# Performance work log

Hardware: AMD Instinct MI355X
Metric: run time of the kernel (lower is better)

## Reference

```python
import jax, jax.numpy as jnp
import numpy as np

B, SQ, SKV, D, H = 2, 2048, 2048, 1024, 16
DH = D // H


def setup_inputs() -> dict:
    key = jax.random.key(0)
    ks = jax.random.split(key, 4)
    s = 0.02
    return {
        "query_input": jax.random.normal(ks[0], (B, SQ, D), jnp.float32),
        "kv_input": jax.random.normal(ks[1], (B, SKV, D), jnp.float32),
        "Wq": jax.random.normal(ks[2], (D, D), jnp.float32) * s,
        "bq": jnp.zeros((D,), jnp.float32),
        "Wkv": jax.random.normal(ks[3], (D, 2 * D), jnp.float32) * s,
        "bkv": jnp.zeros((2 * D,), jnp.float32),
        "Wo": jax.random.normal(jax.random.fold_in(key, 7), (D, D), jnp.float32) * s,
        "bo": jnp.zeros((D,), jnp.float32),
    }


def reference(query_input, kv_input, Wq, bq, Wkv, bkv, Wo, bo):
    scale = 1.0 / jnp.sqrt(jnp.float32(DH))
    # Projections
    q = query_input @ Wq + bq                      # [B, SQ, D]
    kv = kv_input @ Wkv + bkv                      # [B, SKV, 2D]
    k, v = jnp.split(kv, 2, axis=-1)               # [B, SKV, D] each
    # Split heads: [B, H, S, DH]
    q = q.reshape(B, SQ, H, DH).transpose(0, 2, 1, 3)
    k = k.reshape(B, SKV, H, DH).transpose(0, 2, 1, 3)
    v = v.reshape(B, SKV, H, DH).transpose(0, 2, 1, 3)
    # Scores S = QK^T / sqrt(d_k)
    scores = jnp.einsum("bhqd,bhkd->bhqk", q, k) * scale
    attn = jax.nn.softmax(scores, axis=-1)
    out = jnp.einsum("bhqk,bhkd->bhqd", attn, v)   # [B, H, SQ, DH]
    out = out.transpose(0, 2, 1, 3).reshape(B, SQ, D)
    return out @ Wo + bo
```

## Files before the change

### kernel.cpp

```cpp
#include <hip/hip_runtime.h>

typedef unsigned short u16;
typedef unsigned int u32;
typedef __bf16 bf16x8 __attribute__((ext_vector_type(8)));
typedef __bf16 bf16x2 __attribute__((ext_vector_type(2)));
typedef float f32x4 __attribute__((ext_vector_type(4)));

#define QSCALE 0.18033688011112f

__device__ __forceinline__ u16 f2bf(float f) {
  u32 u = __builtin_bit_cast(u32, f);
  u += 0x7fffu + ((u >> 16) & 1u);
  return (u16)(u >> 16);
}

__device__ __forceinline__ u32 pkbf(float a, float b) {
  bf16x2 t = {(__bf16)a, (__bf16)b};
  return __builtin_bit_cast(u32, t);
}

__device__ __forceinline__ float bf2f(u16 x) {
  u32 u = (u32)x << 16;
  return __builtin_bit_cast(float, u);
}

__device__ __forceinline__ bf16x8 as_bf16x8(uint4 v) {
  return __builtin_bit_cast(bf16x8, v);
}

__device__ __forceinline__ void async16(const void* g, void* l) {
  __builtin_amdgcn_global_load_lds(
      (__attribute__((address_space(1))) void*)(g),
      (__attribute__((address_space(3))) void*)(l), 16, 0, 0);
}

__global__ void prep_kernel(const float* __restrict__ xq, const float* __restrict__ xkv,
                            const float* __restrict__ Wq, const float* __restrict__ Wkv,
                            const float* __restrict__ Wo,
                            u16* __restrict__ Xq16, u16* __restrict__ Xkv16,
                            u16* __restrict__ WqT, u16* __restrict__ WkvT,
                            u16* __restrict__ WoT) {
  const int bid = blockIdx.x, tid = threadIdx.x;
  if (bid < 8192) {
    int i = bid * 256 + tid;
    const float* s; u16* d; int j;
    if (i < 1048576) { s = xq; d = Xq16; j = i; }
    else             { s = xkv; d = Xkv16; j = i - 1048576; }
    float4 v = ((const float4*)s)[j];
    ushort4 o;
    o.x = f2bf(v.x); o.y = f2bf(v.y); o.z = f2bf(v.z); o.w = f2bf(v.w);
    ((ushort4*)d)[j] = o;
    return;
  }
  const int b2 = bid - 8192;
  const int z = b2 >> 11, rem = b2 & 2047;
  const int by = rem >> 6, bx = rem & 63;
  const float* src; u16* dst; int Nd;
  if (z == 0)      { src = Wq;  dst = WqT;  Nd = 1024; }
  else if (z == 1) { src = Wkv; dst = WkvT; Nd = 2048; }
  else             { src = Wo;  dst = WoT;  Nd = 1024; }
  const int n0 = bx * 32, k0 = by * 32;
  if (n0 >= Nd) return;
  __shared__ float tile[32][33];
  const int tx = tid & 31, ty = tid >> 5;
#pragma unroll
  for (int j = 0; j < 4; ++j)
    tile[ty + 8 * j][tx] = src[(size_t)(k0 + ty + 8 * j) * Nd + n0 + tx];
  __syncthreads();
#pragma unroll
  for (int j = 0; j < 4; ++j)
    dst[(size_t)(n0 + ty + 8 * j) * 1024 + k0 + tx] = f2bf(tile[tx][ty + 8 * j]);
}

template <int MI>
static __device__ __forceinline__ void gemm_core(
    const u16* __restrict__ A, const u16* __restrict__ Bt, int m0,
    uint4* sA, uint4* sB, f32x4 (*acc)[4]) {
  const int tid = threadIdx.x;
  const int wv = tid >> 6, lane = tid & 63;
  const int quad = lane >> 4, l16 = lane & 15;
  const int wm = (wv >> 1) * (MI * 16), wn = (wv & 1) * 64;

  const int ib0 = wv * 128 + lane, ib1 = ib0 + 64;
  const int br0 = ib0 >> 2, bc0 = (ib0 & 3) ^ ((br0 >> 1) & 3);
  const int br1 = ib1 >> 2, bc1 = (ib1 & 3) ^ ((br1 >> 1) & 3);
  const u16* gB0 = Bt + (size_t)br0 * 1024 + bc0 * 8;
  const u16* gB1 = Bt + (size_t)br1 * 1024 + bc1 * 8;

  const int ia0 = wv * (MI * 32) + lane;
  const int ar0 = ia0 >> 2, ac0 = (ia0 & 3) ^ ((ar0 >> 1) & 3);
  const u16* gA0 = A + (size_t)(m0 + ar0) * 1024 + ac0 * 8;
  const int ia1 = ia0 + 64;
  const int ar1 = ia1 >> 2, ac1 = (ia1 & 3) ^ ((ar1 >> 1) & 3);
  const u16* gA1 = A + (size_t)(m0 + ar1) * 1024 + ac1 * 8;
  uint4* sAw = sA + wv * (MI * 32);
  uint4* sBw = sB + wv * 128;

  for (int k0 = 0; k0 < 1024; k0 += 32) {
    __syncthreads();
    async16(gA0 + k0, sAw);
    if (MI == 4) async16(gA1 + k0, sAw + 64);
    async16(gB0 + k0, sBw);
    async16(gB1 + k0, sBw + 64);
    __syncthreads();

    bf16x8 af[MI], bfr[4];
#pragma unroll
    for (int mi = 0; mi < MI; ++mi) {
      int r = wm + mi * 16 + l16;
      af[mi] = as_bf16x8(sA[r * 4 + (quad ^ ((r >> 1) & 3))]);
    }
#pragma unroll
    for (int ni = 0; ni < 4; ++ni) {
      int r = wn + ni * 16 + l16;
      bfr[ni] = as_bf16x8(sB[r * 4 + (quad ^ ((r >> 1) & 3))]);
    }
#pragma unroll
    for (int mi = 0; mi < MI; ++mi)
#pragma unroll
      for (int ni = 0; ni < 4; ++ni)
        acc[mi][ni] = __builtin_amdgcn_mfma_f32_16x16x32_bf16(
            af[mi], bfr[ni], acc[mi][ni], 0, 0, 0);
  }
}

__global__ __launch_bounds__(256, 3) void gemm_qkv(
    const u16* __restrict__ Xq, const u16* __restrict__ Xkv,
    const u16* __restrict__ WqT, const u16* __restrict__ WkvT,
    const float* __restrict__ bq, const float* __restrict__ bkv,
    u16* __restrict__ Qd, u16* __restrict__ Kd, u16* __restrict__ Vd) {
  __shared__ uint4 sA[512], sB[512];
  f32x4 acc[4][4] = {};
  const int n0 = blockIdx.x * 128, m0 = blockIdx.y * 128;
  const u16* A = (n0 < 1024) ? Xq : Xkv;
  const u16* Bt = (n0 < 1024) ? (WqT + (size_t)n0 * 1024)
                              : (WkvT + (size_t)(n0 - 1024) * 1024);
  const float* bias = (n0 < 1024) ? (bq + n0) : (bkv + (n0 - 1024));
  gemm_core<4>(A, Bt, m0, sA, sB, acc);

  const int tid = threadIdx.x, wv = tid >> 6, lane = tid & 63;
  const int quad = lane >> 4, l16 = lane & 15;
  const int wm = (wv >> 1) * 64, wn = (wv & 1) * 64;
  const int bb = m0 >> 11;
  const int gmb = m0 + wm + quad * 4;
  const int ssb = (m0 & 2047) + wm + quad * 4;
#pragma unroll
  for (int ni = 0; ni < 4; ++ni) {
    const int gn = n0 + wn + ni * 16 + l16;
    const float bvn = bias[wn + ni * 16 + l16];
    if (gn < 1024) {
      u16* base = Qd + gn;
#pragma unroll
      for (int mi = 0; mi < 4; ++mi)
#pragma unroll
        for (int r = 0; r < 4; ++r)
          base[(size_t)(gmb + mi * 16 + r) * 1024] = f2bf((acc[mi][ni][r] + bvn) * QSCALE);
    } else if (gn < 2048) {
      u16* base = Kd + (gn - 1024);
#pragma unroll
      for (int mi = 0; mi < 4; ++mi)
#pragma unroll
        for (int r = 0; r < 4; ++r)
          base[(size_t)(gmb + mi * 16 + r) * 1024] = f2bf(acc[mi][ni][r] + bvn);
    } else {
      const int col = gn - 2048, hh = col >> 6, dh = col & 63;
      u16* base = Vd + ((size_t)(bb * 16 + hh) * 64 + dh) * 2048 + ssb;
#pragma unroll
      for (int mi = 0; mi < 4; ++mi) {
        ushort4 o;
        o.x = f2bf(acc[mi][ni][0] + bvn);
        o.y = f2bf(acc[mi][ni][1] + bvn);
        o.z = f2bf(acc[mi][ni][2] + bvn);
        o.w = f2bf(acc[mi][ni][3] + bvn);
        *(ushort4*)(base + mi * 16) = o;
      }
    }
  }
}

__global__ __launch_bounds__(256, 3) void flash_attn(
    const u16* __restrict__ Q, const u16* __restrict__ K,
    const u16* __restrict__ V, u16* __restrict__ Op,
    float* __restrict__ Lp) {
  __shared__ uint4 sK[2][512];
  __shared__ uint4 sV[2][512];
  __shared__ __align__(16) u16 sP[4][16][72];

  const int tid = threadIdx.x;
  const int wv = tid >> 6, lane = tid & 63;
  const int quad = lane >> 4, l16 = lane & 15;
  const int q0 = blockIdx.x * 128;
  const int h = blockIdx.y;
  const int bz = blockIdx.z >> 1, split = blockIdx.z & 1;
  const int kv0 = split * 1024;

  const u16* Qb = Q + ((size_t)(bz * 2048 + q0)) * 1024 + h * 64;
  const u16* Kb = K + ((size_t)(bz * 2048 + kv0)) * 1024 + h * 64;
  const u16* Vb = V + ((size_t)(bz * 16 + h)) * 64 * 2048 + kv0;

  bf16x8 qf[2][2];
#pragma unroll
  for (int rb = 0; rb < 2; ++rb) {
    const uint4* qp = (const uint4*)(Qb + (size_t)(wv * 32 + rb * 16 + l16) * 1024);
    qf[rb][0] = as_bf16x8(qp[quad]);
    qf[rb][1] = as_bf16x8(qp[4 + quad]);
  }

  f32x4 oacc[2][4] = {};
  f32x4 lsum[2] = {};
  const uint4 ones4 = {0x3F803F80u, 0x3F803F80u, 0x3F803F80u, 0x3F803F80u};
  const bf16x8 ones = as_bf16x8(ones4);

  const int i0 = wv * 128 + lane, i1 = i0 + 64;
  const int kr0 = i0 >> 3, kr1 = i1 >> 3;
  const int kck0 = (i0 & 7) ^ ((i0 >> 5) & 7);
  const int kck1 = (i1 & 7) ^ ((i1 >> 5) & 7);
  const int vck0 = (i0 & 7) ^ (kr0 & 7);
  const int vck1 = (i1 & 7) ^ (kr1 & 7);
  const u16* gK0 = Kb + (size_t)kr0 * 1024 + kck0 * 8;
  const u16* gK1 = Kb + (size_t)kr1 * 1024 + kck1 * 8;
  const u16* gV0 = Vb + (size_t)kr0 * 2048 + vck0 * 8;
  const u16* gV1 = Vb + (size_t)kr1 * 2048 + vck1 * 8;
  const int wo = wv * 128;

  async16(gK0, &sK[0][wo]);
  async16(gK1, &sK[0][wo + 64]);
  async16(gV0, &sV[0][wo]);
  async16(gV1, &sV[0][wo + 64]);

  for (int t = 0; t < 16; ++t) {
    const int cur = t & 1;
    __syncthreads();
    if (t < 15) {
      const int nxt = cur ^ 1;
      const size_t ko = (size_t)(t + 1) * 64 * 1024;
      const int vo = (t + 1) * 64;
      async16(gK0 + ko, &sK[nxt][wo]);
      async16(gK1 + ko, &sK[nxt][wo + 64]);
      async16(gV0 + vo, &sV[nxt][wo]);
      async16(gV1 + vo, &sV[nxt][wo + 64]);
    }
    const uint4* K_ = sK[cur];
    const uint4* V_ = sV[cur];

    bf16x8 bK0[4], bK1[4], vf0[4], vf1[4];
#pragma unroll
    for (int ni = 0; ni < 4; ++ni) {
      int rr = l16 * 4 + ni;
      bK0[ni] = as_bf16x8(K_[rr * 8 + (quad ^ (l16 & 7))]);
      bK1[ni] = as_bf16x8(K_[rr * 8 + ((4 + quad) ^ (l16 & 7))]);
      int vv = ni * 16 + l16;
      vf0[ni] = as_bf16x8(V_[vv * 8 + (quad ^ (vv & 7))]);
      vf1[ni] = as_bf16x8(V_[vv * 8 + ((4 + quad) ^ (vv & 7))]);
    }

#pragma unroll
    for (int rb = 0; rb < 2; ++rb) {
      f32x4 s4[4];
#pragma unroll
      for (int ni = 0; ni < 4; ++ni) {
        f32x4 a = {0.f, 0.f, 0.f, 0.f};
        a = __builtin_amdgcn_mfma_f32_16x16x32_bf16(qf[rb][0], bK0[ni], a, 0, 0, 0);
        a = __builtin_amdgcn_mfma_f32_16x16x32_bf16(qf[rb][1], bK1[ni], a, 0, 0, 0);
        s4[ni] = a;
      }
#pragma unroll
      for (int r = 0; r < 4; ++r) {
        uint2 pk;
        pk.x = pkbf(exp2f(s4[0][r]), exp2f(s4[1][r]));
        pk.y = pkbf(exp2f(s4[2][r]), exp2f(s4[3][r]));
        *(uint2*)&sP[wv][quad * 4 + r][l16 * 4] = pk;
      }
      bf16x8 pf0 = as_bf16x8(*(const uint4*)&sP[wv][l16][quad * 8]);
      bf16x8 pf1 = as_bf16x8(*(const uint4*)&sP[wv][l16][32 + quad * 8]);
      lsum[rb] = __builtin_amdgcn_mfma_f32_16x16x32_bf16(pf0, ones, lsum[rb], 0, 0, 0);
      lsum[rb] = __builtin_amdgcn_mfma_f32_16x16x32_bf16(pf1, ones, lsum[rb], 0, 0, 0);
#pragma unroll
      for (int ni = 0; ni < 4; ++ni) {
        oacc[rb][ni] = __builtin_amdgcn_mfma_f32_16x16x32_bf16(pf0, vf0[ni], oacc[rb][ni], 0, 0, 0);
        oacc[rb][ni] = __builtin_amdgcn_mfma_f32_16x16x32_bf16(pf1, vf1[ni], oacc[rb][ni], 0, 0, 0);
      }
    }
  }

#pragma unroll
  for (int rb = 0; rb < 2; ++rb) {
    const int row = bz * 2048 + q0 + wv * 32 + rb * 16 + quad * 4;
    u16* Ob = Op + ((size_t)split * 4096 + row) * 1024 + h * 64;
#pragma unroll
    for (int r = 0; r < 4; ++r)
#pragma unroll
      for (int ni = 0; ni < 4; ++ni)
        Ob[(size_t)r * 1024 + ni * 16 + l16] = f2bf(oacc[rb][ni][r]);
    if (l16 == 0)
#pragma unroll
      for (int r = 0; r < 4; ++r)
        Lp[((size_t)split * 4096 + row + r) * 16 + h] = lsum[rb][r];
  }
}

__global__ void combine_kernel(const u16* __restrict__ Op,
                               const float* __restrict__ Lp,
                               u16* __restrict__ O16) {
  const int row = blockIdx.x, t = threadIdx.x;
  const int h = t >> 4;
  const float rl = 1.0f / (Lp[(size_t)row * 16 + h] + Lp[(size_t)(4096 + row) * 16 + h]);
  ushort4 a = ((const ushort4*)(Op + (size_t)row * 1024))[t];
  ushort4 b = ((const ushort4*)(Op + (size_t)(4096 + row) * 1024))[t];
  ushort4 o;
  o.x = f2bf((bf2f(a.x) + bf2f(b.x)) * rl);
  o.y = f2bf((bf2f(a.y) + bf2f(b.y)) * rl);
  o.z = f2bf((bf2f(a.z) + bf2f(b.z)) * rl);
  o.w = f2bf((bf2f(a.w) + bf2f(b.w)) * rl);
  ((ushort4*)(O16 + (size_t)row * 1024))[t] = o;
}

__global__ __launch_bounds__(256, 2) void gemm_out(
    const u16* __restrict__ A, const u16* __restrict__ Bt,
    const float* __restrict__ bias, float* __restrict__ C) {
  __shared__ uint4 sA[256], sB[512];
  f32x4 acc[2][4] = {};
  const int n0 = blockIdx.x * 128, m0 = blockIdx.y * 64;
  gemm_core<2>(A, Bt + (size_t)n0 * 1024, m0, sA, sB, acc);

  const int tid = threadIdx.x, wv = tid >> 6, lane = tid & 63;
  const int quad = lane >> 4, l16 = lane & 15;
  const int wm = (wv >> 1) * 32, wn = (wv & 1) * 64;
  float bv[4];
#pragma unroll
  for (int ni = 0; ni < 4; ++ni) bv[ni] = bias[n0 + wn + ni * 16 + l16];
#pragma unroll
  for (int mi = 0; mi < 2; ++mi)
#pragma unroll
    for (int ni = 0; ni < 4; ++ni)
#pragma unroll
      for (int r = 0; r < 4; ++r) {
        int gm = m0 + wm + mi * 16 + quad * 4 + r;
        int gn = n0 + wn + ni * 16 + l16;
        C[(size_t)gm * 1024 + gn] = acc[mi][ni][r] + bv[ni];
      }
}

extern "C" void kernel_launch(void* const* d_in, const int* in_sizes, int n_in,
                              void* d_out, int out_size, void* d_ws, size_t ws_size,
                              hipStream_t stream) {
  const float* xq  = (const float*)d_in[0];
  const float* xkv = (const float*)d_in[1];
  const float* Wq  = (const float*)d_in[2];
  const float* bq  = (const float*)d_in[3];
  const float* Wkv = (const float*)d_in[4];
  const float* bkv = (const float*)d_in[5];
  const float* Wo  = (const float*)d_in[6];
  const float* bo  = (const float*)d_in[7];
  float* out = (float*)d_out;

  char* p = (char*)d_ws;
  u16* Xq16  = (u16*)p; p += (size_t)8 << 20;
  u16* Xkv16 = (u16*)p; p += (size_t)8 << 20;
  u16* WqT   = (u16*)p; p += (size_t)2 << 20;
  u16* WkvT  = (u16*)p; p += (size_t)4 << 20;
  u16* WoT   = (u16*)p; p += (size_t)2 << 20;
  u16* Q16   = (u16*)p; p += (size_t)8 << 20;
  u16* K16   = (u16*)p; p += (size_t)8 << 20;
  u16* Vt16  = (u16*)p; p += (size_t)8 << 20;
  u16* O16   = (u16*)p; p += (size_t)8 << 20;
  u16* Op    = Xq16;
  float* Lp  = (float*)WqT;

  prep_kernel<<<14336, 256, 0, stream>>>(xq, xkv, Wq, Wkv, Wo,
                                         Xq16, Xkv16, WqT, WkvT, WoT);
  gemm_qkv<<<dim3(24, 32), 256, 0, stream>>>(Xq16, Xkv16, WqT, WkvT, bq, bkv,
                                             Q16, K16, Vt16);
  flash_attn<<<dim3(16, 16, 4), 256, 0, stream>>>(Q16, K16, Vt16, Op, Lp);
  combine_kernel<<<4096, 256, 0, stream>>>(Op, Lp, O16);
  gemm_out<<<dim3(8, 64), 256, 0, stream>>>(O16, WoT, bo, out);
}
```

Before: 223.1 us.

## Remove split-KV in flash attention and normalize in-kernel, dropping combine pass

Flash attention now processes the full 2048-length KV range per block instead of splitting it in two, so the softmax normalization is done directly in the epilogue and the separate combine kernel and partial-output round trip are removed. The grid goes from 1024 to 512 blocks with a linearized index that groups head/batch together, and occupancy hint drops from 3 to 2. The P staging buffer is enlarged so both row blocks write P before the PV MFMAs, separating exp and PV phases. Fewer blocks risks lower parallelism on a large CU count, but saves a launch and extra memory traffic.

```diff
diff --git a/kernel.cpp b/kernel.cpp
--- a/kernel.cpp
+++ b/kernel.cpp
@@ -17,11 +17,6 @@
 __device__ __forceinline__ u32 pkbf(float a, float b) {
   bf16x2 t = {(__bf16)a, (__bf16)b};
   return __builtin_bit_cast(u32, t);
-}
-
-__device__ __forceinline__ float bf2f(u16 x) {
-  u32 u = (u32)x << 16;
-  return __builtin_bit_cast(float, u);
 }
 
 __device__ __forceinline__ bf16x8 as_bf16x8(uint4 v) {
@@ -178,25 +173,23 @@
   }
 }
 
-__global__ __launch_bounds__(256, 3) void flash_attn(
+__global__ __launch_bounds__(256, 2) void flash_attn(
     const u16* __restrict__ Q, const u16* __restrict__ K,
-    const u16* __restrict__ V, u16* __restrict__ Op,
-    float* __restrict__ Lp) {
+    const u16* __restrict__ V, u16* __restrict__ O) {
   __shared__ uint4 sK[2][512];
   __shared__ uint4 sV[2][512];
-  __shared__ __align__(16) u16 sP[4][16][72];
+  __shared__ __align__(16) u16 sP[4][32][72];
 
   const int tid = threadIdx.x;
   const int wv = tid >> 6, lane = tid & 63;
   const int quad = lane >> 4, l16 = lane & 15;
-  const int q0 = blockIdx.x * 128;
-  const int h = blockIdx.y;
-  const int bz = blockIdx.z >> 1, split = blockIdx.z & 1;
-  const int kv0 = split * 1024;
+  const int hb = blockIdx.x & 31;
+  const int q0 = (blockIdx.x >> 5) * 128;
+  const int h = hb & 15, bz = hb >> 4;
 
   const u16* Qb = Q + ((size_t)(bz * 2048 + q0)) * 1024 + h * 64;
-  const u16* Kb = K + ((size_t)(bz * 2048 + kv0)) * 1024 + h * 64;
-  const u16* Vb = V + ((size_t)(bz * 16 + h)) * 64 * 2048 + kv0;
+  const u16* Kb = K + ((size_t)(bz * 2048)) * 1024 + h * 64;
+  const u16* Vb = V + ((size_t)(bz * 16 + h)) * 64 * 2048;
 
   bf16x8 qf[2][2];
 #pragma unroll
@@ -228,10 +221,10 @@
   async16(gV0, &sV[0][wo]);
   async16(gV1, &sV[0][wo + 64]);
 
-  for (int t = 0; t < 16; ++t) {
+  for (int t = 0; t < 32; ++t) {
     const int cur = t & 1;
     __syncthreads();
-    if (t < 15) {
+    if (t < 31) {
       const int nxt = cur ^ 1;
       const size_t ko = (size_t)(t + 1) * 64 * 1024;
       const int vo = (t + 1) * 64;
@@ -269,10 +262,13 @@
         uint2 pk;
         pk.x = pkbf(exp2f(s4[0][r]), exp2f(s4[1][r]));
         pk.y = pkbf(exp2f(s4[2][r]), exp2f(s4[3][r]));
-        *(uint2*)&sP[wv][quad * 4 + r][l16 * 4] = pk;
-      }
-      bf16x8 pf0 = as_bf16x8(*(const uint4*)&sP[wv][l16][quad * 8]);
-      bf16x8 pf1 = as_bf16x8(*(const uint4*)&sP[wv][l16][32 + quad * 8]);
+        *(uint2*)&sP[wv][rb * 16 + quad * 4 + r][l16 * 4] = pk;
+      }
+    }
+#pragma unroll
+    for (int rb = 0; rb < 2; ++rb) {
+      bf16x8 pf0 = as_bf16x8(*(const uint4*)&sP[wv][rb * 16 + l16][quad * 8]);
+      bf16x8 pf1 = as_bf16x8(*(const uint4*)&sP[wv][rb * 16 + l16][32 + quad * 8]);
       lsum[rb] = __builtin_amdgcn_mfma_f32_16x16x32_bf16(pf0, ones, lsum[rb], 0, 0, 0);
       lsum[rb] = __builtin_amdgcn_mfma_f32_16x16x32_bf16(pf1, ones, lsum[rb], 0, 0, 0);
 #pragma unroll
@@ -285,34 +281,16 @@
 
 #pragma unroll
   for (int rb = 0; rb < 2; ++rb) {
-    const int row = bz * 2048 + q0 + wv * 32 + rb * 16 + quad * 4;
-    u16* Ob = Op + ((size_t)split * 4096 + row) * 1024 + h * 64;
-#pragma unroll
-    for (int r = 0; r < 4; ++r)
+    u16* Ob = O + ((size_t)(bz * 2048 + q0 + wv * 32 + rb * 16 + quad * 4)) * 1024
+                + h * 64;
+#pragma unroll
+    for (int r = 0; r < 4; ++r) {
+      float rl = 1.0f / lsum[rb][r];
 #pragma unroll
       for (int ni = 0; ni < 4; ++ni)
-        Ob[(size_t)r * 1024 + ni * 16 + l16] = f2bf(oacc[rb][ni][r]);
-    if (l16 == 0)
-#pragma unroll
-      for (int r = 0; r < 4; ++r)
-        Lp[((size_t)split * 4096 + row + r) * 16 + h] = lsum[rb][r];
-  }
-}
-
-__global__ void combine_kernel(const u16* __restrict__ Op,
-                               const float* __restrict__ Lp,
-                               u16* __restrict__ O16) {
-  const int row = blockIdx.x, t = threadIdx.x;
-  const int h = t >> 4;
-  const float rl = 1.0f / (Lp[(size_t)row * 16 + h] + Lp[(size_t)(4096 + row) * 16 + h]);
-  ushort4 a = ((const ushort4*)(Op + (size_t)row * 1024))[t];
-  ushort4 b = ((const ushort4*)(Op + (size_t)(4096 + row) * 1024))[t];
-  ushort4 o;
-  o.x = f2bf((bf2f(a.x) + bf2f(b.x)) * rl);
-  o.y = f2bf((bf2f(a.y) + bf2f(b.y)) * rl);
-  o.z = f2bf((bf2f(a.z) + bf2f(b.z)) * rl);
-  o.w = f2bf((bf2f(a.w) + bf2f(b.w)) * rl);
-  ((ushort4*)(O16 + (size_t)row * 1024))[t] = o;
+        Ob[(size_t)r * 1024 + ni * 16 + l16] = f2bf(oacc[rb][ni][r] * rl);
+    }
+  }
 }
 
 __global__ __launch_bounds__(256, 2) void gemm_out(
@@ -364,14 +342,11 @@
   u16* K16   = (u16*)p; p += (size_t)8 << 20;
   u16* Vt16  = (u16*)p; p += (size_t)8 << 20;
   u16* O16   = (u16*)p; p += (size_t)8 << 20;
-  u16* Op    = Xq16;
-  float* Lp  = (float*)WqT;
 
   prep_kernel<<<14336, 256, 0, stream>>>(xq, xkv, Wq, Wkv, Wo,
                                          Xq16, Xkv16, WqT, WkvT, WoT);
   gemm_qkv<<<dim3(24, 32), 256, 0, stream>>>(Xq16, Xkv16, WqT, WkvT, bq, bkv,
                                              Q16, K16, Vt16);
-  flash_attn<<<dim3(16, 16, 4), 256, 0, stream>>>(Q16, K16, Vt16, Op, Lp);
-  combine_kernel<<<4096, 256, 0, stream>>>(Op, Lp, O16);
+  flash_attn<<<512, 256, 0, stream>>>(Q16, K16, Vt16, O16);
   gemm_out<<<dim3(8, 64), 256, 0, stream>>>(O16, WoT, bo, out);
 }
```

Result: faster. 210.8 us (-5.5%).
